# Performance work log

Hardware: AMD Instinct MI355X
Metric: run time of the kernel (lower is better)

The kernel has to match this reference:

```python
import jax, jax.numpy as jnp
import numpy as np

NEG_SLOPE = 0.2  # PyG GATConv default leaky_relu slope


def gat_conv(x, src, dst, W, att_s, att_d, bias, concat):
    """Single PyG-style GATConv (eval mode, self-loops already in src/dst).
    x: [N, F_in]; W: [F_in, H*D]; att_s, att_d: [H, D]; bias: [H*D] or [D]."""
    N = x.shape[0]
    H, D = att_s.shape
    h = (x @ W).reshape(N, H, D)                      # [N,H,D]
    a_s = (h * att_s[None]).sum(-1)                   # [N,H]
    a_d = (h * att_d[None]).sum(-1)                   # [N,H]
    e = a_s[src] + a_d[dst]                           # [E,H]
    e = jnp.where(e > 0, e, NEG_SLOPE * e)            # leaky_relu
    # edge softmax over incoming edges of each destination node
    m = jax.ops.segment_max(e, dst, num_segments=N)
    m = jnp.where(jnp.isfinite(m), m, 0.0)
    ex = jnp.exp(e - m[dst])
    denom = jax.ops.segment_sum(ex, dst, num_segments=N)
    alpha = ex / (denom[dst] + 1e-16)                 # [E,H]
    out = jax.ops.segment_sum(alpha[:, :, None] * h[src], dst, num_segments=N)  # [N,H,D]
    out = out.reshape(N, H * D) if concat else out.mean(axis=1)
    return out + bias


def setup_inputs() -> dict:
    key = jax.random.key(0)
    ks = jax.random.split(key, 16)
    B, N, E, F = 4, 4096, 131072, 768
    HID, HEADS, C = 64, 4, 6
    s = 0.05
    inp = {
        'node_feat': jax.random.normal(ks[0], (B, N, F), jnp.float32),
        'labels': jax.random.randint(ks[1], (B,), 0, C, jnp.int32),
        'edge_index': jax.random.randint(ks[2], (B, 2, E), 0, N, jnp.int32),
        'W1': jax.random.normal(ks[3], (F, HEADS * HID), jnp.float32) * s,
        'as1': jax.random.normal(ks[4], (HEADS, HID), jnp.float32) * s,
        'ad1': jax.random.normal(ks[5], (HEADS, HID), jnp.float32) * s,
        'b1': jnp.zeros((HEADS * HID,), jnp.float32),
        'W2': jax.random.normal(ks[6], (HEADS * HID, HEADS * HID), jnp.float32) * s,
        'as2': jax.random.normal(ks[7], (HEADS, HID), jnp.float32) * s,
        'ad2': jax.random.normal(ks[8], (HEADS, HID), jnp.float32) * s,
        'b2': jnp.zeros((HEADS * HID,), jnp.float32),
        # gat3: 256 -> 64, 1 head, mean (concat=False)
        'W3': jax.random.normal(ks[9], (HEADS * HID, HID), jnp.float32) * s,
        'as3': jax.random.normal(ks[10], (1, HID), jnp.float32) * s,
        'ad3': jax.random.normal(ks[11], (1, HID), jnp.float32) * s,
        'b3': jnp.zeros((HID,), jnp.float32),
        # classifier
        'Wc': jax.random.normal(ks[12], (HID, C), jnp.float32) * s,
        'bc': jnp.zeros((C,), jnp.float32),
    }
    return inp


def reference(node_feat, labels, edge_index, W1, as1, ad1, b1, W2, as2, ad2, b2, W3, as3, ad3, b3, Wc, bc):
    B, N, _ = node_feat.shape
    loops = jnp.arange(N, dtype=edge_index.dtype)

    def single_graph(x, ei):
        # PyG GATConv adds self-loops by default
        src = jnp.concatenate([ei[0], loops])
        dst = jnp.concatenate([ei[1], loops])
        h = jax.nn.elu(gat_conv(x, src, dst, W1, as1, ad1, b1, True))
        h = jax.nn.elu(gat_conv(h, src, dst, W2, as2, ad2, b2, True))
        h = gat_conv(h, src, dst, W3, as3, ad3, b3, False)
        graph_embed = h.mean(axis=0)                  # [HID]
        return graph_embed @ Wc + bc                  # [C]

    logits = jax.vmap(single_graph)(node_feat, edge_index)   # [B,C]
    logp = jax.nn.log_softmax(logits, axis=-1)
    loss = -logp[jnp.arange(B), labels].mean()
    pred = jnp.argmax(logits, axis=1)
    return (pred, labels, loss)
```

## Files before the change

kernel.cpp:

```cpp
#include <hip/hip_runtime.h>
#include <math.h>

#define B_ 4
#define N_ 4096
#define E_ 131072
#define ET_ (E_ + N_)
#define H_ 4
#define HD_ 256
#define C_ 6

typedef short  s16x8  __attribute__((ext_vector_type(8)));
typedef __bf16 bf16x8 __attribute__((ext_vector_type(8)));
typedef float  f32x4  __attribute__((ext_vector_type(4)));

__device__ inline unsigned short f2bf(float f){
  unsigned u = __builtin_bit_cast(unsigned, f);
  return (unsigned short)((u + 0x7FFFu + ((u >> 16) & 1u)) >> 16);
}
__device__ inline float bf2f(unsigned short s){
  unsigned u = ((unsigned)s) << 16;
  return __builtin_bit_cast(float, u);
}
__device__ inline float bflo(unsigned u){ return __builtin_bit_cast(float, u << 16); }
__device__ inline float bfhi(unsigned u){ return __builtin_bit_cast(float, u & 0xFFFF0000u); }
__device__ inline void split2(float f, short& hi, short& lo){
  unsigned short h = f2bf(f);
  hi = (short)h;
  lo = (short)f2bf(f - bf2f(h));
}
__device__ inline f32x4 mfma_bf16(s16x8 a, s16x8 b, f32x4 c){
  return __builtin_amdgcn_mfma_f32_16x16x32_bf16(
      __builtin_bit_cast(bf16x8, a), __builtin_bit_cast(bf16x8, b), c, 0, 0, 0);
}

__global__ void k_count(const int* __restrict__ ei, int* __restrict__ counts){
  int idx = blockIdx.x*256 + threadIdx.x;
  if (idx >= B_*ET_) return;
  int b = idx / ET_, i = idx - b*ET_;
  int dst = (i < E_) ? ei[b*2*E_ + E_ + i] : (i - E_);
  atomicAdd(&counts[b*N_ + dst], 1);
}

__global__ void k_scan(const int* __restrict__ counts, int* __restrict__ offs){
  __shared__ int lds[1024];
  int b = blockIdx.x, t = threadIdx.x;
  int c[4]; int tot = 0;
  #pragma unroll
  for (int j=0;j<4;j++){ c[j] = counts[b*N_ + t*4 + j]; tot += c[j]; }
  lds[t] = tot; __syncthreads();
  for (int off=1; off<1024; off<<=1){
    int u = (t>=off) ? lds[t-off] : 0;
    __syncthreads();
    lds[t] += u;
    __syncthreads();
  }
  int excl = lds[t] - tot;
  int o = excl;
  #pragma unroll
  for (int j=0;j<4;j++){ offs[b*(N_+1) + t*4 + j] = o; o += c[j]; }
  if (t==1023) offs[b*(N_+1) + N_] = o;
}

__global__ void k_scatter(const int* __restrict__ ei, const int* __restrict__ offs,
                          int* __restrict__ cursor, unsigned short* __restrict__ srcs){
  int idx = blockIdx.x*256 + threadIdx.x;
  if (idx >= B_*ET_) return;
  int b = idx / ET_, i = idx - b*ET_;
  int src, dst;
  if (i < E_){ src = ei[b*2*E_ + i]; dst = ei[b*2*E_ + E_ + i]; }
  else { src = i - E_; dst = src; }
  int pos = offs[b*(N_+1) + dst] + atomicAdd(&cursor[b*N_ + dst], 1);
  srcs[b*ET_ + pos] = (unsigned short)src;
}

__global__ void k_splitT(const float* __restrict__ w, short* __restrict__ hit,
                         short* __restrict__ lot, int K, int NC){
  int idx = blockIdx.x*256 + threadIdx.x;
  if (idx >= K*NC) return;
  int nn = idx / K, kk = idx - nn*K;
  float f = w[(size_t)kk*NC + nn];
  short h, l; split2(f, h, l);
  hit[idx] = h; lot[idx] = l;
}

template<int K, bool AFP32, int H>
__global__ __launch_bounds__(256) void k_mfma(const float* __restrict__ Af,
    const short* __restrict__ Ah, const short* __restrict__ Al,
    const short* __restrict__ Bh, const short* __restrict__ Bl,
    unsigned short* __restrict__ Ob, int NC,
    const float* __restrict__ atts, const float* __restrict__ attd,
    float* __restrict__ a_s, float* __restrict__ a_d){
  __shared__ short tAh[64][32], tAl[64][32], tBh[64][32], tBl[64][32];
  int t = threadIdx.x;
  int m0 = blockIdx.x*64, n0 = blockIdx.y*64;
  int head = blockIdx.y;
  int r = t >> 2, c = t & 3;
  int cs = (c ^ ((r >> 1) & 3)) * 8;
  int w = t >> 6, l = t & 63;
  int wr = w >> 1, wc = w & 1, g = l >> 4, li = l & 15;
  int rA = wr*32 + li, rB = wc*32 + li;
  int cA = (g ^ ((rA >> 1) & 3)) * 8;
  int cB = (g ^ ((rB >> 1) & 3)) * 8;
  f32x4 z = {0.f,0.f,0.f,0.f};
  f32x4 acc00=z, acc01=z, acc10=z, acc11=z;

  s16x8 vah, vaL, vbh, vbl;
  auto loadSlice = [&](int k0){
    if constexpr (AFP32){
      const float* ap = &Af[(size_t)(m0+r)*K + k0 + c*8];
      float4 f0 = *reinterpret_cast<const float4*>(ap);
      float4 f1 = *reinterpret_cast<const float4*>(ap+4);
      float fv[8] = {f0.x,f0.y,f0.z,f0.w,f1.x,f1.y,f1.z,f1.w};
      #pragma unroll
      for (int j=0;j<8;j++){ short hh,ll; split2(fv[j],hh,ll); vah[j]=hh; vaL[j]=ll; }
    } else {
      vah = *reinterpret_cast<const s16x8*>(&Ah[(size_t)(m0+r)*K + k0 + c*8]);
      vaL = *reinterpret_cast<const s16x8*>(&Al[(size_t)(m0+r)*K + k0 + c*8]);
    }
    vbh = *reinterpret_cast<const s16x8*>(&Bh[(size_t)(n0+r)*K + k0 + c*8]);
    vbl = *reinterpret_cast<const s16x8*>(&Bl[(size_t)(n0+r)*K + k0 + c*8]);
  };

  loadSlice(0);
  for (int k0 = 0; k0 < K; k0 += 32){
    __syncthreads();
    *reinterpret_cast<s16x8*>(&tAh[r][cs]) = vah;
    *reinterpret_cast<s16x8*>(&tAl[r][cs]) = vaL;
    *reinterpret_cast<s16x8*>(&tBh[r][cs]) = vbh;
    *reinterpret_cast<s16x8*>(&tBl[r][cs]) = vbl;
    __syncthreads();
    if (k0 + 32 < K) loadSlice(k0 + 32);
    s16x8 a0h = *reinterpret_cast<const s16x8*>(&tAh[rA   ][cA]);
    s16x8 a1h = *reinterpret_cast<const s16x8*>(&tAh[rA+16][cA]);
    s16x8 a0l = *reinterpret_cast<const s16x8*>(&tAl[rA   ][cA]);
    s16x8 a1l = *reinterpret_cast<const s16x8*>(&tAl[rA+16][cA]);
    s16x8 b0h = *reinterpret_cast<const s16x8*>(&tBh[rB   ][cB]);
    s16x8 b1h = *reinterpret_cast<const s16x8*>(&tBh[rB+16][cB]);
    s16x8 b0l = *reinterpret_cast<const s16x8*>(&tBl[rB   ][cB]);
    s16x8 b1l = *reinterpret_cast<const s16x8*>(&tBl[rB+16][cB]);
    acc00 = mfma_bf16(a0h, b0h, acc00);
    acc00 = mfma_bf16(a0h, b0l, acc00);
    acc00 = mfma_bf16(a0l, b0h, acc00);
    acc01 = mfma_bf16(a0h, b1h, acc01);
    acc01 = mfma_bf16(a0h, b1l, acc01);
    acc01 = mfma_bf16(a0l, b1h, acc01);
    acc10 = mfma_bf16(a1h, b0h, acc10);
    acc10 = mfma_bf16(a1h, b0l, acc10);
    acc10 = mfma_bf16(a1l, b0h, acc10);
    acc11 = mfma_bf16(a1h, b1h, acc11);
    acc11 = mfma_bf16(a1h, b1l, acc11);
    acc11 = mfma_bf16(a1l, b1h, acc11);
  }
  f32x4 accs[2][2] = {{acc00, acc01},{acc10, acc11}};
  float attsv[2], attdv[2];
  #pragma unroll
  for (int ni=0; ni<2; ni++){
    int colg = n0 + wc*32 + ni*16 + li;
    attsv[ni] = atts[colg];
    attdv[ni] = attd[colg];
  }
  #pragma unroll
  for (int mi=0; mi<2; mi++){
    #pragma unroll
    for (int j=0; j<4; j++){
      int row = m0 + wr*32 + mi*16 + 4*g + j;
      float sa = accs[mi][0][j]*attsv[0] + accs[mi][1][j]*attsv[1];
      float sd = accs[mi][0][j]*attdv[0] + accs[mi][1][j]*attdv[1];
      #pragma unroll
      for (int m=1; m<16; m<<=1){ sa += __shfl_xor(sa,m,64); sd += __shfl_xor(sd,m,64); }
      if (li == 0){
        atomicAdd(&a_s[(size_t)row*H + head], sa);
        atomicAdd(&a_d[(size_t)row*H + head], sd);
      }
      #pragma unroll
      for (int ni=0; ni<2; ni++){
        int col = n0 + wc*32 + ni*16 + li;
        Ob[(size_t)row*NC + col] = f2bf(accs[mi][ni][j]);
      }
    }
  }
}

template<int HD, int H, bool ELU, bool SPLIT>
__global__ __launch_bounds__(256) void k_aggr(const unsigned short* __restrict__ h,
    const float* __restrict__ a_s, const float* __restrict__ a_d,
    const unsigned short* __restrict__ srcs, const int* __restrict__ offs,
    const float* __restrict__ bias, float* __restrict__ outf,
    short* __restrict__ outh, short* __restrict__ outl){
  constexpr int EPW = (HD==256) ? 2 : 4;
  constexpr int LPE = 64/EPW;
  constexpr int CPL = HD/LPE;
  constexpr int NP  = 4*EPW;
  __shared__ float accL[NP][HD];
  __shared__ float psumL[NP][H];
  int ng = blockIdx.x;
  int b = ng >> 12, n = ng & (N_-1);
  int t = threadIdx.x;
  int w = t >> 6, l = t & 63;
  int sub = l / LPE, hl = l % LPE;
  int slot = w*EPW + sub;
  int st = offs[b*(N_+1)+n], en = offs[b*(N_+1)+n+1];
  const unsigned short* sp = &srcs[(size_t)b*ET_];
  const unsigned short* hb = &h[(size_t)b*N_*HD];
  const float* asb = &a_s[(size_t)b*N_*H];
  int head = (H==4) ? ((hl*CPL) >> 6) : 0;
  float adv = a_d[(size_t)ng*H + head];
  float acc[CPL];
  #pragma unroll
  for (int j=0;j<CPL;j++) acc[j]=0.f;
  float psum = 0.f;

  auto ldh = [&](int s, float* dst){
    const unsigned short* p = &hb[(size_t)s*HD + hl*CPL];
    if constexpr (CPL==8){
      uint4 q = *reinterpret_cast<const uint4*>(p);
      dst[0]=bflo(q.x); dst[1]=bfhi(q.x); dst[2]=bflo(q.y); dst[3]=bfhi(q.y);
      dst[4]=bflo(q.z); dst[5]=bfhi(q.z); dst[6]=bflo(q.w); dst[7]=bfhi(q.w);
    } else {
      uint2 q = *reinterpret_cast<const uint2*>(p);
      dst[0]=bflo(q.x); dst[1]=bfhi(q.x); dst[2]=bflo(q.y); dst[3]=bfhi(q.y);
    }
  };

  int i  = st + slot;
  int s0 = (i      < en) ? (int)sp[i]      : 0;
  int s1 = (i+NP   < en) ? (int)sp[i+NP]   : 0;
  float hv[CPL], hn[CPL], asv, asn;
  ldh(s0, hv); asv = asb[s0*H + head];

  while (i < en){
    int s2 = (i+2*NP < en) ? (int)sp[i+2*NP] : 0;
    ldh(s1, hn); asn = asb[s1*H + head];
    float e = asv + adv;
    e = fmaxf(e, 0.2f*e);
    float p = __expf(e);
    #pragma unroll
    for (int j=0;j<CPL;j++) acc[j] = fmaf(p, hv[j], acc[j]);
    psum += p;
    #pragma unroll
    for (int j=0;j<CPL;j++) hv[j] = hn[j];
    asv = asn; s1 = s2; i += NP;
  }

  #pragma unroll
  for (int j=0;j<CPL;j+=4)
    *reinterpret_cast<float4*>(&accL[slot][hl*CPL+j]) =
        make_float4(acc[j],acc[j+1],acc[j+2],acc[j+3]);
  if constexpr (H==4){ if ((hl & 7)==0) psumL[slot][hl>>3] = psum; }
  else               { if (hl == 0)     psumL[slot][0]     = psum; }
  __syncthreads();
  if (t < HD){
    float a = 0.f;
    #pragma unroll
    for (int k=0;k<NP;k++) a += accL[k][t];
    int h2 = (H==4) ? (t>>6) : 0;
    float ps = 0.f;
    #pragma unroll
    for (int k=0;k<NP;k++) ps += psumL[k][h2];
    float val = a/(ps + 1e-16f) + bias[t];
    if (ELU) val = val > 0.f ? val : expm1f(val);
    size_t idx = (size_t)ng*HD + t;
    if (SPLIT){ short hh, ll; split2(val, hh, ll); outh[idx]=hh; outl[idx]=ll; }
    else outf[idx] = val;
  }
}

__global__ void k_reduce(const float* __restrict__ x3, float* __restrict__ embed){
  __shared__ float red[256];
  int bid = blockIdx.x; int b = bid>>4, chunk = bid & 15;
  int t = threadIdx.x; int col = t & 63, q = t>>6;
  float s = 0.f;
  int r0 = chunk*256 + q*64;
  const float* p = &x3[((size_t)b*N_ + r0)*64 + col];
  for (int j=0;j<64;j++) s += p[(size_t)j*64];
  red[t]=s; __syncthreads();
  if (t<64){
    float v = red[t]+red[t+64]+red[t+128]+red[t+192];
    atomicAdd(&embed[b*64+t], v);
  }
}

__global__ void k_final(const float* __restrict__ embed, const float* __restrict__ Wc,
                        const float* __restrict__ bc, const int* __restrict__ labels,
                        float* __restrict__ out){
  __shared__ float lg[B_][C_];
  __shared__ float lossv[B_];
  int t = threadIdx.x;
  if (t < B_*C_){
    int b = t / C_, c = t - b*C_;
    float s = 0.f;
    for (int k=0;k<64;k++) s += embed[b*64+k]*Wc[k*C_+c];
    lg[b][c] = s*(1.0f/N_) + bc[c];
  }
  __syncthreads();
  if (t < B_){
    int b = t;
    float mx = lg[b][0]; int pred = 0;
    for (int c=1;c<C_;c++) if (lg[b][c] > mx){ mx = lg[b][c]; pred = c; }
    float se = 0.f;
    for (int c=0;c<C_;c++) se += expf(lg[b][c]-mx);
    float lse = mx + logf(se);
    int lab = labels[b];
    lossv[b] = lse - lg[b][lab];
    out[b]      = (float)pred;
    out[B_+b]   = (float)lab;
  }
  __syncthreads();
  if (t==0) out[8] = 0.25f*(lossv[0]+lossv[1]+lossv[2]+lossv[3]);
}

extern "C" void kernel_launch(void* const* d_in, const int* in_sizes, int n_in,
                              void* d_out, int out_size, void* d_ws, size_t ws_size,
                              hipStream_t stream){
  const float* x0     = (const float*)d_in[0];
  const int*   labels = (const int*)d_in[1];
  const int*   ei     = (const int*)d_in[2];
  const float* W1=(const float*)d_in[3],  *as1=(const float*)d_in[4],
             *ad1=(const float*)d_in[5],  *b1 =(const float*)d_in[6];
  const float* W2=(const float*)d_in[7],  *as2=(const float*)d_in[8],
             *ad2=(const float*)d_in[9],  *b2 =(const float*)d_in[10];
  const float* W3=(const float*)d_in[11], *as3=(const float*)d_in[12],
             *ad3=(const float*)d_in[13], *b3 =(const float*)d_in[14];
  const float* Wc=(const float*)d_in[15], *bc =(const float*)d_in[16];
  float* out = (float*)d_out;

  char* ws = (char*)d_ws;
  size_t off = 0;
  auto alloc = [&](size_t bytes)->void*{ void* p = ws + off; off += (bytes + 255) & ~(size_t)255; return p; };
  unsigned short* hbuf = (unsigned short*)alloc((size_t)B_*N_*HD_*2);
  float* xcur3  = (float*)alloc((size_t)B_*N_*64*4);
  int*   counts = (int*)alloc((size_t)B_*N_*4);
  int*   cursor = (int*)alloc((size_t)B_*N_*4);
  int*   offs   = (int*)alloc((size_t)B_*(N_+1)*4);
  unsigned short* srcs = (unsigned short*)alloc((size_t)B_*ET_*2);
  float* embed  = (float*)alloc((size_t)B_*64*4);
  float* a_s1   = (float*)alloc((size_t)B_*N_*H_*4);
  float* a_d1   = (float*)alloc((size_t)B_*N_*H_*4);
  float* a_s2   = (float*)alloc((size_t)B_*N_*H_*4);
  float* a_d2   = (float*)alloc((size_t)B_*N_*H_*4);
  float* a_s3   = (float*)alloc((size_t)B_*N_*4);
  float* a_d3   = (float*)alloc((size_t)B_*N_*4);
  size_t zend   = off;
  short* Ah     = (short*)alloc((size_t)B_*N_*HD_*2);
  short* Al     = (short*)alloc((size_t)B_*N_*HD_*2);
  short* Wht    = (short*)alloc((size_t)768*256*2);
  short* Wlt    = (short*)alloc((size_t)768*256*2);

  hipMemsetAsync(counts, 0, (size_t)B_*N_*4*2, stream);
  hipMemsetAsync(embed,  0, zend - ((char*)embed - ws), stream);

  int nb = (B_*ET_ + 255)/256;
  k_count  <<<nb, 256, 0, stream>>>(ei, counts);
  k_scan   <<<B_, 1024, 0, stream>>>(counts, offs);
  k_scatter<<<nb, 256, 0, stream>>>(ei, offs, cursor, srcs);

  {
    k_splitT<<<(768*256+255)/256, 256, 0, stream>>>(W1, Wht, Wlt, 768, 256);
    k_mfma<768,true,4><<<dim3(B_*N_/64, 4), 256, 0, stream>>>(x0, nullptr, nullptr,
        Wht, Wlt, hbuf, 256, as1, ad1, a_s1, a_d1);
    k_aggr<256,4,true,true><<<B_*N_, 256, 0, stream>>>(hbuf, a_s1, a_d1, srcs, offs, b1,
                                                       nullptr, Ah, Al);
  }
  {
    k_splitT<<<(256*256+255)/256, 256, 0, stream>>>(W2, Wht, Wlt, 256, 256);
    k_mfma<256,false,4><<<dim3(B_*N_/64, 4), 256, 0, stream>>>(nullptr, Ah, Al,
        Wht, Wlt, hbuf, 256, as2, ad2, a_s2, a_d2);
    k_aggr<256,4,true,true><<<B_*N_, 256, 0, stream>>>(hbuf, a_s2, a_d2, srcs, offs, b2,
                                                       nullptr, Ah, Al);
  }
  {
    k_splitT<<<(256*64+255)/256, 256, 0, stream>>>(W3, Wht, Wlt, 256, 64);
    k_mfma<256,false,1><<<dim3(B_*N_/64, 1), 256, 0, stream>>>(nullptr, Ah, Al,
        Wht, Wlt, hbuf, 64, as3, ad3, a_s3, a_d3);
    k_aggr<64,1,false,false><<<B_*N_, 256, 0, stream>>>(hbuf, a_s3, a_d3, srcs, offs, b3,
                                                        xcur3, nullptr, nullptr);
  }

  k_reduce<<<B_*16, 256, 0, stream>>>(xcur3, embed);
  k_final <<<1, 64, 0, stream>>>(embed, Wc, bc, labels, out);
}
```

Before: 341.0 us.

## Use 128x128 tiled MFMA GEMM for the two wide GAT projection layers

Adds a new GEMM kernel with 128x128 output tiles, where each wave computes a 64x64 sub-tile using 4x4 MFMA fragments. It is used for layers 1 and 2, and the attention logits for two heads per block are fused into the epilogue. The larger tile reuses each loaded A/B slice across more MFMAs, which cuts global and LDS traffic per FLOP. In exchange it uses more registers and runs only 256 blocks, which may hurt occupancy and latency hiding.

```diff
diff --git a/kernel.cpp b/kernel.cpp
--- a/kernel.cpp
+++ b/kernel.cpp
@@ -84,7 +84,118 @@
 }
 
 template<int K, bool AFP32, int H>
-__global__ __launch_bounds__(256) void k_mfma(const float* __restrict__ Af,
+__global__ __launch_bounds__(256,1) void k_gemm_b(const float* __restrict__ Af,
+    const short* __restrict__ Ah_, const short* __restrict__ Al_,
+    const short* __restrict__ Bh_, const short* __restrict__ Bl_,
+    unsigned short* __restrict__ Ob, int NC,
+    const float* __restrict__ atts, const float* __restrict__ attd,
+    float* __restrict__ a_s, float* __restrict__ a_d){
+  __shared__ short tAh[128][32], tAl[128][32], tBh[128][32], tBl[128][32];
+  int t = threadIdx.x;
+  int m0 = blockIdx.x*128, n0 = blockIdx.y*128;
+  int w = t >> 6, l = t & 63;
+  int wrow = w >> 1, wcol = w & 1, g = l >> 4, li = l & 15;
+  int sr = t >> 2, sq = t & 3;
+
+  s16x8 sAh[2], sAl[2], sBh[2], sBl[2];
+  auto stageLoad = [&](int k0){
+    #pragma unroll
+    for (int hh=0; hh<2; hh++){
+      int r = sr + hh*64;
+      if constexpr (AFP32){
+        const float* ap = &Af[(size_t)(m0+r)*K + k0 + sq*8];
+        float4 f0 = *reinterpret_cast<const float4*>(ap);
+        float4 f1 = *reinterpret_cast<const float4*>(ap+4);
+        float fv[8] = {f0.x,f0.y,f0.z,f0.w,f1.x,f1.y,f1.z,f1.w};
+        #pragma unroll
+        for (int j=0;j<8;j++){ short hi,lo; split2(fv[j],hi,lo); sAh[hh][j]=hi; sAl[hh][j]=lo; }
+      } else {
+        sAh[hh] = *reinterpret_cast<const s16x8*>(&Ah_[(size_t)(m0+r)*K + k0 + sq*8]);
+        sAl[hh] = *reinterpret_cast<const s16x8*>(&Al_[(size_t)(m0+r)*K + k0 + sq*8]);
+      }
+      sBh[hh] = *reinterpret_cast<const s16x8*>(&Bh_[(size_t)(n0+r)*K + k0 + sq*8]);
+      sBl[hh] = *reinterpret_cast<const s16x8*>(&Bl_[(size_t)(n0+r)*K + k0 + sq*8]);
+    }
+  };
+
+  f32x4 acc[4][4];
+  #pragma unroll
+  for (int mi=0;mi<4;mi++)
+    #pragma unroll
+    for (int ni=0;ni<4;ni++) acc[mi][ni] = f32x4{0.f,0.f,0.f,0.f};
+
+  int fcs = (g ^ ((li>>1)&3)) * 8;
+
+  stageLoad(0);
+  for (int k0 = 0; k0 < K; k0 += 32){
+    __syncthreads();
+    #pragma unroll
+    for (int hh=0; hh<2; hh++){
+      int r = sr + hh*64;
+      int cs = (sq ^ ((r>>1)&3)) * 8;
+      *reinterpret_cast<s16x8*>(&tAh[r][cs]) = sAh[hh];
+      *reinterpret_cast<s16x8*>(&tAl[r][cs]) = sAl[hh];
+      *reinterpret_cast<s16x8*>(&tBh[r][cs]) = sBh[hh];
+      *reinterpret_cast<s16x8*>(&tBl[r][cs]) = sBl[hh];
+    }
+    __syncthreads();
+    if (k0 + 32 < K) stageLoad(k0 + 32);
+    s16x8 ah[4], al[4], bh[4], bl[4];
+    #pragma unroll
+    for (int mi=0;mi<4;mi++){
+      int rA = wrow*64 + mi*16 + li;
+      ah[mi] = *reinterpret_cast<const s16x8*>(&tAh[rA][fcs]);
+      al[mi] = *reinterpret_cast<const s16x8*>(&tAl[rA][fcs]);
+    }
+    #pragma unroll
+    for (int ni=0;ni<4;ni++){
+      int rB = wcol*64 + ni*16 + li;
+      bh[ni] = *reinterpret_cast<const s16x8*>(&tBh[rB][fcs]);
+      bl[ni] = *reinterpret_cast<const s16x8*>(&tBl[rB][fcs]);
+    }
+    #pragma unroll
+    for (int mi=0;mi<4;mi++)
+      #pragma unroll
+      for (int ni=0;ni<4;ni++){
+        acc[mi][ni] = mfma_bf16(ah[mi], bh[ni], acc[mi][ni]);
+        acc[mi][ni] = mfma_bf16(ah[mi], bl[ni], acc[mi][ni]);
+        acc[mi][ni] = mfma_bf16(al[mi], bh[ni], acc[mi][ni]);
+      }
+  }
+
+  int head = blockIdx.y*2 + wcol;
+  float attsv[4], attdv[4];
+  #pragma unroll
+  for (int ni=0;ni<4;ni++){
+    int col = n0 + wcol*64 + ni*16 + li;
+    attsv[ni] = atts[col]; attdv[ni] = attd[col];
+  }
+  #pragma unroll
+  for (int mi=0;mi<4;mi++){
+    #pragma unroll
+    for (int j=0;j<4;j++){
+      int row = m0 + wrow*64 + mi*16 + 4*g + j;
+      float sa = acc[mi][0][j]*attsv[0] + acc[mi][1][j]*attsv[1]
+               + acc[mi][2][j]*attsv[2] + acc[mi][3][j]*attsv[3];
+      float sd = acc[mi][0][j]*attdv[0] + acc[mi][1][j]*attdv[1]
+               + acc[mi][2][j]*attdv[2] + acc[mi][3][j]*attdv[3];
+      #pragma unroll
+      for (int m=1;m<16;m<<=1){ sa += __shfl_xor(sa,m,64); sd += __shfl_xor(sd,m,64); }
+      if (li == 0){
+        a_s[(size_t)row*H + head] = sa;
+        a_d[(size_t)row*H + head] = sd;
+      }
+      #pragma unroll
+      for (int ni=0;ni<4;ni++){
+        int col = n0 + wcol*64 + ni*16 + li;
+        Ob[(size_t)row*NC + col] = f2bf(acc[mi][ni][j]);
+      }
+    }
+  }
+}
+
+template<int K, bool AFP32, int H>
+__global__ __launch_bounds__(256) void k_gemm_s(const float* __restrict__ Af,
     const short* __restrict__ Ah, const short* __restrict__ Al,
     const short* __restrict__ Bh, const short* __restrict__ Bl,
     unsigned short* __restrict__ Ob, int NC,
@@ -106,17 +217,8 @@
 
   s16x8 vah, vaL, vbh, vbl;
   auto loadSlice = [&](int k0){
-    if constexpr (AFP32){
-      const float* ap = &Af[(size_t)(m0+r)*K + k0 + c*8];
-      float4 f0 = *reinterpret_cast<const float4*>(ap);
-      float4 f1 = *reinterpret_cast<const float4*>(ap+4);
-      float fv[8] = {f0.x,f0.y,f0.z,f0.w,f1.x,f1.y,f1.z,f1.w};
-      #pragma unroll
-      for (int j=0;j<8;j++){ short hh,ll; split2(fv[j],hh,ll); vah[j]=hh; vaL[j]=ll; }
-    } else {
-      vah = *reinterpret_cast<const s16x8*>(&Ah[(size_t)(m0+r)*K + k0 + c*8]);
-      vaL = *reinterpret_cast<const s16x8*>(&Al[(size_t)(m0+r)*K + k0 + c*8]);
-    }
+    vah = *reinterpret_cast<const s16x8*>(&Ah[(size_t)(m0+r)*K + k0 + c*8]);
+    vaL = *reinterpret_cast<const s16x8*>(&Al[(size_t)(m0+r)*K + k0 + c*8]);
     vbh = *reinterpret_cast<const s16x8*>(&Bh[(size_t)(n0+r)*K + k0 + c*8]);
     vbl = *reinterpret_cast<const s16x8*>(&Bl[(size_t)(n0+r)*K + k0 + c*8]);
   };
@@ -356,21 +458,21 @@
 
   {
     k_splitT<<<(768*256+255)/256, 256, 0, stream>>>(W1, Wht, Wlt, 768, 256);
-    k_mfma<768,true,4><<<dim3(B_*N_/64, 4), 256, 0, stream>>>(x0, nullptr, nullptr,
+    k_gemm_b<768,true,4><<<dim3(B_*N_/128, 2), 256, 0, stream>>>(x0, nullptr, nullptr,
         Wht, Wlt, hbuf, 256, as1, ad1, a_s1, a_d1);
     k_aggr<256,4,true,true><<<B_*N_, 256, 0, stream>>>(hbuf, a_s1, a_d1, srcs, offs, b1,
                                                        nullptr, Ah, Al);
   }
   {
     k_splitT<<<(256*256+255)/256, 256, 0, stream>>>(W2, Wht, Wlt, 256, 256);
-    k_mfma<256,false,4><<<dim3(B_*N_/64, 4), 256, 0, stream>>>(nullptr, Ah, Al,
+    k_gemm_b<256,false,4><<<dim3(B_*N_/128, 2), 256, 0, stream>>>(nullptr, Ah, Al,
         Wht, Wlt, hbuf, 256, as2, ad2, a_s2, a_d2);
     k_aggr<256,4,true,true><<<B_*N_, 256, 0, stream>>>(hbuf, a_s2, a_d2, srcs, offs, b2,
                                                        nullptr, Ah, Al);
   }
   {
     k_splitT<<<(256*64+255)/256, 256, 0, stream>>>(W3, Wht, Wlt, 256, 64);
-    k_mfma<256,false,1><<<dim3(B_*N_/64, 1), 256, 0, stream>>>(nullptr, Ah, Al,
+    k_gemm_s<256,false,1><<<dim3(B_*N_/64, 1), 256, 0, stream>>>(nullptr, Ah, Al,
         Wht, Wlt, hbuf, 64, as3, ad3, a_s3, a_d3);
     k_aggr<64,1,false,false><<<B_*N_, 256, 0, stream>>>(hbuf, a_s3, a_d3, srcs, offs, b3,
                                                         xcur3, nullptr, nullptr);
```

Result: faster. 333.6 us (-2.2%).

## Replace LDS-tiled GEMM with register-resident per-wave 64x64 tiles

Applied to the files above, without the earlier changes.

The shared-memory 64x64 block GEMM is replaced by a kernel where each wave owns a full 64x64 output tile. Operands are loaded straight from global memory into registers with software double buffering, which removes the LDS staging and the block barriers. Because one wave now covers all 64 columns of a head, the attention logits are written with plain stores instead of atomics. The cost is much higher register pressure (launch_bounds 256,1), 4x fewer blocks, and reliance on cache for operand reuse across waves.

```diff
diff --git a/kernel.cpp b/kernel.cpp
--- a/kernel.cpp
+++ b/kernel.cpp
@@ -84,98 +84,118 @@
 }
 
 template<int K, bool AFP32, int H>
-__global__ __launch_bounds__(256) void k_mfma(const float* __restrict__ Af,
-    const short* __restrict__ Ah, const short* __restrict__ Al,
-    const short* __restrict__ Bh, const short* __restrict__ Bl,
+__global__ __launch_bounds__(256,1) void k_gemm_r(const float* __restrict__ Af,
+    const short* __restrict__ Ah_, const short* __restrict__ Al_,
+    const short* __restrict__ Bh_, const short* __restrict__ Bl_,
     unsigned short* __restrict__ Ob, int NC,
     const float* __restrict__ atts, const float* __restrict__ attd,
     float* __restrict__ a_s, float* __restrict__ a_d){
-  __shared__ short tAh[64][32], tAl[64][32], tBh[64][32], tBl[64][32];
   int t = threadIdx.x;
-  int m0 = blockIdx.x*64, n0 = blockIdx.y*64;
+  int w = t >> 6, l = t & 63, g = l >> 4, li = l & 15;
+  int m0 = (blockIdx.x*4 + w)*64;
+  int n0 = blockIdx.y*64;
   int head = blockIdx.y;
-  int r = t >> 2, c = t & 3;
-  int cs = (c ^ ((r >> 1) & 3)) * 8;
-  int w = t >> 6, l = t & 63;
-  int wr = w >> 1, wc = w & 1, g = l >> 4, li = l & 15;
-  int rA = wr*32 + li, rB = wc*32 + li;
-  int cA = (g ^ ((rA >> 1) & 3)) * 8;
-  int cB = (g ^ ((rB >> 1) & 3)) * 8;
-  f32x4 z = {0.f,0.f,0.f,0.f};
-  f32x4 acc00=z, acc01=z, acc10=z, acc11=z;
-
-  s16x8 vah, vaL, vbh, vbl;
-  auto loadSlice = [&](int k0){
-    if constexpr (AFP32){
-      const float* ap = &Af[(size_t)(m0+r)*K + k0 + c*8];
-      float4 f0 = *reinterpret_cast<const float4*>(ap);
-      float4 f1 = *reinterpret_cast<const float4*>(ap+4);
-      float fv[8] = {f0.x,f0.y,f0.z,f0.w,f1.x,f1.y,f1.z,f1.w};
+
+  size_t offB[4], offA[4];
+  #pragma unroll
+  for (int ni=0;ni<4;ni++) offB[ni] = (size_t)(n0 + ni*16 + li)*K + g*8;
+  #pragma unroll
+  for (int mi=0;mi<4;mi++) offA[mi] = (size_t)(m0 + mi*16 + li)*K + g*8;
+
+  f32x4 acc[4][4];
+  #pragma unroll
+  for (int mi=0;mi<4;mi++)
+    #pragma unroll
+    for (int ni=0;ni<4;ni++) acc[mi][ni] = f32x4{0.f,0.f,0.f,0.f};
+
+  s16x8 bhc[4], blc[4], bhn[4], bln[4];
+  s16x8 ahc[4], alc[4], ahn[4], aln[4];
+  float4 a0c[4], a1c[4], a0n[4], a1n[4];
+
+  auto loadB = [&](int k0, s16x8* bh, s16x8* bl){
+    #pragma unroll
+    for (int ni=0;ni<4;ni++){
+      bh[ni] = *reinterpret_cast<const s16x8*>(Bh_ + offB[ni] + k0);
+      bl[ni] = *reinterpret_cast<const s16x8*>(Bl_ + offB[ni] + k0);
+    }
+  };
+  auto loadA = [&](int k0, s16x8* ah, s16x8* al, float4* a0, float4* a1){
+    #pragma unroll
+    for (int mi=0;mi<4;mi++){
+      if constexpr (AFP32){
+        const float* ap = Af + offA[mi] + k0;
+        a0[mi] = *reinterpret_cast<const float4*>(ap);
+        a1[mi] = *reinterpret_cast<const float4*>(ap+4);
+      } else {
+        ah[mi] = *reinterpret_cast<const s16x8*>(Ah_ + offA[mi] + k0);
+        al[mi] = *reinterpret_cast<const s16x8*>(Al_ + offA[mi] + k0);
+      }
+    }
+  };
+
+  loadB(0, bhc, blc);
+  loadA(0, ahc, alc, a0c, a1c);
+
+  for (int k0 = 0; k0 < K; k0 += 32){
+    bool more = (k0 + 32 < K);
+    if (more){
+      loadB(k0+32, bhn, bln);
+      loadA(k0+32, ahn, aln, a0n, a1n);
+    }
+    s16x8 ah[4], al[4];
+    #pragma unroll
+    for (int mi=0;mi<4;mi++){
+      if constexpr (AFP32){
+        float fv[8] = {a0c[mi].x,a0c[mi].y,a0c[mi].z,a0c[mi].w,
+                       a1c[mi].x,a1c[mi].y,a1c[mi].z,a1c[mi].w};
+        #pragma unroll
+        for (int j=0;j<8;j++){ short hi,lo; split2(fv[j],hi,lo); ah[mi][j]=hi; al[mi][j]=lo; }
+      } else { ah[mi] = ahc[mi]; al[mi] = alc[mi]; }
+    }
+    #pragma unroll
+    for (int mi=0;mi<4;mi++)
       #pragma unroll
-      for (int j=0;j<8;j++){ short hh,ll; split2(fv[j],hh,ll); vah[j]=hh; vaL[j]=ll; }
-    } else {
-      vah = *reinterpret_cast<const s16x8*>(&Ah[(size_t)(m0+r)*K + k0 + c*8]);
-      vaL = *reinterpret_cast<const s16x8*>(&Al[(size_t)(m0+r)*K + k0 + c*8]);
-    }
-    vbh = *reinterpret_cast<const s16x8*>(&Bh[(size_t)(n0+r)*K + k0 + c*8]);
-    vbl = *reinterpret_cast<const s16x8*>(&Bl[(size_t)(n0+r)*K + k0 + c*8]);
-  };
-
-  loadSlice(0);
-  for (int k0 = 0; k0 < K; k0 += 32){
-    __syncthreads();
-    *reinterpret_cast<s16x8*>(&tAh[r][cs]) = vah;
-    *reinterpret_cast<s16x8*>(&tAl[r][cs]) = vaL;
-    *reinterpret_cast<s16x8*>(&tBh[r][cs]) = vbh;
-    *reinterpret_cast<s16x8*>(&tBl[r][cs]) = vbl;
-    __syncthreads();
-    if (k0 + 32 < K) loadSlice(k0 + 32);
-    s16x8 a0h = *reinterpret_cast<const s16x8*>(&tAh[rA   ][cA]);
-    s16x8 a1h = *reinterpret_cast<const s16x8*>(&tAh[rA+16][cA]);
-    s16x8 a0l = *reinterpret_cast<const s16x8*>(&tAl[rA   ][cA]);
-    s16x8 a1l = *reinterpret_cast<const s16x8*>(&tAl[rA+16][cA]);
-    s16x8 b0h = *reinterpret_cast<const s16x8*>(&tBh[rB   ][cB]);
-    s16x8 b1h = *reinterpret_cast<const s16x8*>(&tBh[rB+16][cB]);
-    s16x8 b0l = *reinterpret_cast<const s16x8*>(&tBl[rB   ][cB]);
-    s16x8 b1l = *reinterpret_cast<const s16x8*>(&tBl[rB+16][cB]);
-    acc00 = mfma_bf16(a0h, b0h, acc00);
-    acc00 = mfma_bf16(a0h, b0l, acc00);
-    acc00 = mfma_bf16(a0l, b0h, acc00);
-    acc01 = mfma_bf16(a0h, b1h, acc01);
-    acc01 = mfma_bf16(a0h, b1l, acc01);
-    acc01 = mfma_bf16(a0l, b1h, acc01);
-    acc10 = mfma_bf16(a1h, b0h, acc10);
-    acc10 = mfma_bf16(a1h, b0l, acc10);
-    acc10 = mfma_bf16(a1l, b0h, acc10);
-    acc11 = mfma_bf16(a1h, b1h, acc11);
-    acc11 = mfma_bf16(a1h, b1l, acc11);
-    acc11 = mfma_bf16(a1l, b1h, acc11);
-  }
-  f32x4 accs[2][2] = {{acc00, acc01},{acc10, acc11}};
-  float attsv[2], attdv[2];
-  #pragma unroll
-  for (int ni=0; ni<2; ni++){
-    int colg = n0 + wc*32 + ni*16 + li;
-    attsv[ni] = atts[colg];
-    attdv[ni] = attd[colg];
-  }
-  #pragma unroll
-  for (int mi=0; mi<2; mi++){
-    #pragma unroll
-    for (int j=0; j<4; j++){
-      int row = m0 + wr*32 + mi*16 + 4*g + j;
-      float sa = accs[mi][0][j]*attsv[0] + accs[mi][1][j]*attsv[1];
-      float sd = accs[mi][0][j]*attdv[0] + accs[mi][1][j]*attdv[1];
+      for (int ni=0;ni<4;ni++){
+        acc[mi][ni] = mfma_bf16(ah[mi], bhc[ni], acc[mi][ni]);
+        acc[mi][ni] = mfma_bf16(ah[mi], blc[ni], acc[mi][ni]);
+        acc[mi][ni] = mfma_bf16(al[mi], bhc[ni], acc[mi][ni]);
+      }
+    if (more){
       #pragma unroll
-      for (int m=1; m<16; m<<=1){ sa += __shfl_xor(sa,m,64); sd += __shfl_xor(sd,m,64); }
+      for (int ni=0;ni<4;ni++){ bhc[ni]=bhn[ni]; blc[ni]=bln[ni]; }
+      #pragma unroll
+      for (int mi=0;mi<4;mi++){
+        if constexpr (AFP32){ a0c[mi]=a0n[mi]; a1c[mi]=a1n[mi]; }
+        else { ahc[mi]=ahn[mi]; alc[mi]=aln[mi]; }
+      }
+    }
+  }
+
+  float attsv[4], attdv[4];
+  #pragma unroll
+  for (int ni=0;ni<4;ni++){
+    int col = n0 + ni*16 + li;
+    attsv[ni] = atts[col]; attdv[ni] = attd[col];
+  }
+  #pragma unroll
+  for (int mi=0;mi<4;mi++){
+    #pragma unroll
+    for (int j=0;j<4;j++){
+      int row = m0 + mi*16 + 4*g + j;
+      float sa = acc[mi][0][j]*attsv[0] + acc[mi][1][j]*attsv[1]
+               + acc[mi][2][j]*attsv[2] + acc[mi][3][j]*attsv[3];
+      float sd = acc[mi][0][j]*attdv[0] + acc[mi][1][j]*attdv[1]
+               + acc[mi][2][j]*attdv[2] + acc[mi][3][j]*attdv[3];
+      #pragma unroll
+      for (int m=1;m<16;m<<=1){ sa += __shfl_xor(sa,m,64); sd += __shfl_xor(sd,m,64); }
       if (li == 0){
-        atomicAdd(&a_s[(size_t)row*H + head], sa);
-        atomicAdd(&a_d[(size_t)row*H + head], sd);
+        a_s[(size_t)row*H + head] = sa;
+        a_d[(size_t)row*H + head] = sd;
       }
       #pragma unroll
-      for (int ni=0; ni<2; ni++){
-        int col = n0 + wc*32 + ni*16 + li;
-        Ob[(size_t)row*NC + col] = f2bf(accs[mi][ni][j]);
+      for (int ni=0;ni<4;ni++){
+        int col = n0 + ni*16 + li;
+        Ob[(size_t)row*NC + col] = f2bf(acc[mi][ni][j]);
       }
     }
   }
@@ -356,21 +376,21 @@
 
   {
     k_splitT<<<(768*256+255)/256, 256, 0, stream>>>(W1, Wht, Wlt, 768, 256);
-    k_mfma<768,true,4><<<dim3(B_*N_/64, 4), 256, 0, stream>>>(x0, nullptr, nullptr,
+    k_gemm_r<768,true,4><<<dim3(B_*N_/256, 4), 256, 0, stream>>>(x0, nullptr, nullptr,
         Wht, Wlt, hbuf, 256, as1, ad1, a_s1, a_d1);
     k_aggr<256,4,true,true><<<B_*N_, 256, 0, stream>>>(hbuf, a_s1, a_d1, srcs, offs, b1,
                                                        nullptr, Ah, Al);
   }
   {
     k_splitT<<<(256*256+255)/256, 256, 0, stream>>>(W2, Wht, Wlt, 256, 256);
-    k_mfma<256,false,4><<<dim3(B_*N_/64, 4), 256, 0, stream>>>(nullptr, Ah, Al,
+    k_gemm_r<256,false,4><<<dim3(B_*N_/256, 4), 256, 0, stream>>>(nullptr, Ah, Al,
         Wht, Wlt, hbuf, 256, as2, ad2, a_s2, a_d2);
     k_aggr<256,4,true,true><<<B_*N_, 256, 0, stream>>>(hbuf, a_s2, a_d2, srcs, offs, b2,
                                                        nullptr, Ah, Al);
   }
   {
     k_splitT<<<(256*64+255)/256, 256, 0, stream>>>(W3, Wht, Wlt, 256, 64);
-    k_mfma<256,false,1><<<dim3(B_*N_/64, 1), 256, 0, stream>>>(nullptr, Ah, Al,
+    k_gemm_r<256,false,1><<<dim3(B_*N_/256, 1), 256, 0, stream>>>(nullptr, Ah, Al,
         Wht, Wlt, hbuf, 64, as3, ad3, a_s3, a_d3);
     k_aggr<64,1,false,false><<<B_*N_, 256, 0, stream>>>(hbuf, a_s3, a_d3, srcs, offs, b3,
                                                         xcur3, nullptr, nullptr);
```

Measured after the change: 367.8 us. 1.08x slower.
